# Kernel optimization log

Measured on AMD Instinct MI355X. Metric: run time of the kernel, lower is better.

Reference implementation:

```python
import jax, jax.numpy as jnp
import numpy as np

N = 50000      # nodes
E = 800000     # edges (avg degree 16)
F_IN = 128
H = 128        # hidden_channels
C = 10         # num_classes
S = 5          # Chebyshev order K
B = 8          # graphs in batch


def setup_inputs() -> dict:
    key = jax.random.key(0)
    ks = jax.random.split(key, 9)
    x = jax.random.normal(ks[0], (N, F_IN), jnp.float32)
    edge_index = jax.random.randint(ks[1], (2, E), 0, N, dtype=jnp.int64)
    batch = jnp.sort(jax.random.randint(ks[2], (N,), 0, B, dtype=jnp.int64))
    lambda_max = 2.0 * jnp.ones((B,), jnp.float32)
    W1 = jax.random.normal(ks[3], (S, F_IN, H), jnp.float32) * 0.05
    b1 = jax.random.normal(ks[4], (H,), jnp.float32) * 0.05
    W2 = jax.random.normal(ks[5], (S, H, H), jnp.float32) * 0.05
    b2 = jax.random.normal(ks[6], (H,), jnp.float32) * 0.05
    Wlin = jax.random.normal(ks[7], (H, C), jnp.float32) * 0.05
    blin = jax.random.normal(ks[8], (C,), jnp.float32) * 0.05
    return {"x": x, "edge_index": edge_index, "batch": batch,
            "lambda_max": lambda_max, "W1": W1, "b1": b1,
            "W2": W2, "b2": b2, "Wlin": Wlin, "blin": blin}


def _cheb_conv(x, row, col, w_edge, diag, W, b):
    # scaled Laplacian matvec: L_hat v = scatter(w_edge * v[col] -> row) + diag * v
    def Lhat(v):
        msg = v[col] * w_edge[:, None]                       # [E, d]
        return jax.ops.segment_sum(msg, row, num_segments=N) + diag[:, None] * v

    Tx0 = x
    out = Tx0 @ W[0]
    Tx1 = Lhat(Tx0)
    out = out + Tx1 @ W[1]
    for k in range(2, W.shape[0]):                           # Chebyshev recurrence
        Tx2 = 2.0 * Lhat(Tx1) - Tx0
        out = out + Tx2 @ W[k]
        Tx0, Tx1 = Tx1, Tx2
    return out + b


def reference(x, edge_index, batch, lambda_max, W1, b1, W2, b2, Wlin, blin):
    row, col = edge_index[0], edge_index[1]
    # sym-normalized Laplacian L = I - D^{-1/2} A D^{-1/2}; L_hat = 2L/lambda_max - I
    deg = jax.ops.segment_sum(jnp.ones((E,), x.dtype), row, num_segments=N)
    dis = jnp.where(deg > 0, jax.lax.rsqrt(jnp.maximum(deg, 1e-12)), 0.0)
    lam_e = lambda_max[batch[row]]                           # per-edge lambda_max
    w_edge = -2.0 * dis[row] * dis[col] / lam_e              # off-diagonal of L_hat
    diag = 2.0 / lambda_max[batch] - 1.0                     # diagonal of L_hat per node

    h = jax.nn.relu(_cheb_conv(x, row, col, w_edge, diag, W1, b1))
    h = jax.nn.relu(_cheb_conv(h, row, col, w_edge, diag, W2, b2))

    # global_mean_pool over batch assignment
    sums = jax.ops.segment_sum(h, batch, num_segments=B)     # [B, H]
    counts = jax.ops.segment_sum(jnp.ones((N, 1), h.dtype), batch, num_segments=B)
    pooled = sums / jnp.maximum(counts, 1.0)
    return pooled @ Wlin + blin                              # [B, C] logits (softmax unused in forward)
```

## Files before the change

kernel.cpp:

```cpp
#include <hip/hip_runtime.h>
#include <stdint.h>

typedef __attribute__((ext_vector_type(8))) short bf16x8;
typedef __attribute__((ext_vector_type(4))) float f32x4;

__device__ __forceinline__ float bf16lo_to_f(uint32_t u) { return __uint_as_float(u << 16); }
__device__ __forceinline__ float bf16hi_to_f(uint32_t u) { return __uint_as_float(u & 0xffff0000u); }
__device__ __forceinline__ uint16_t f_to_bf16(float f) {
    uint32_t u = __float_as_uint(f);
    uint32_t r = u + 0x7fff + ((u >> 16) & 1);
    return (uint16_t)(r >> 16);
}


#define BINCH 4096

__global__ void __launch_bounds__(256) k_bhist(const int* __restrict__ row,
                                               int* __restrict__ bhist, int E) {
    __shared__ int sh[256];
    int t = threadIdx.x;
    sh[t] = 0;
    __syncthreads();
    int stride = gridDim.x * blockDim.x;
    for (int e = blockIdx.x * blockDim.x + t; e < E; e += stride)
        atomicAdd(&sh[row[e] >> 8], 1);
    __syncthreads();
    if (sh[t]) atomicAdd(&bhist[t], sh[t]);
}

__global__ void k_bscan(const int* __restrict__ bhist, int* __restrict__ gbase,
                        int* __restrict__ gcur, int nbk) {
    __shared__ int sh[256];
    int t = threadIdx.x;
    int v = t < nbk ? bhist[t] : 0;
    sh[t] = v;
    __syncthreads();
    for (int o = 1; o < 256; o <<= 1) {
        int u = (t >= o) ? sh[t - o] : 0;
        __syncthreads();
        sh[t] += u;
        __syncthreads();
    }
    gbase[t] = sh[t] - v;
    gcur[t] = sh[t] - v;
    if (t == 255) gbase[256] = sh[255];
}

__global__ void __launch_bounds__(256) k_bin(const int* __restrict__ row,
        const int* __restrict__ col, int* __restrict__ gcur,
        uint32_t* __restrict__ bout, int E) {
    __shared__ uint32_t stage[BINCH];
    __shared__ int hist[256], hscan[256], hcur[256], gofs[256];
    int t = threadIdx.x;
    int e0 = blockIdx.x * BINCH;
    int ecnt = min(BINCH, E - e0);
    hist[t] = 0;
    __syncthreads();
    for (int i = t; i < ecnt; i += 256)
        atomicAdd(&hist[row[e0 + i] >> 8], 1);
    __syncthreads();
    int v = hist[t];
    hscan[t] = v;
    __syncthreads();
    for (int o = 1; o < 256; o <<= 1) {
        int u = (t >= o) ? hscan[t - o] : 0;
        __syncthreads();
        hscan[t] += u;
        __syncthreads();
    }
    hcur[t] = hscan[t] - v;
    __syncthreads();
    for (int i = t; i < ecnt; i += 256) {
        int r = row[e0 + i];
        int p = atomicAdd(&hcur[r >> 8], 1);
        stage[p] = (uint32_t)(r & 255) | ((uint32_t)col[e0 + i] << 8);
    }
    __syncthreads();
    if (v > 0) gofs[t] = atomicAdd(&gcur[t], v);
    __syncthreads();
    for (int i = t; i < ecnt; i += 256) {
        int lo = 0, hi = 255;
        while (lo < hi) { int mid = (lo + hi) >> 1; if (hscan[mid] > i) hi = mid; else lo = mid + 1; }
        int b = lo;
        int local = i - (hscan[b] - hist[b]);
        bout[gofs[b] + local] = stage[i];
    }
}

__global__ void __launch_bounds__(256) k_deg2(const uint32_t* __restrict__ bout,
        const int* __restrict__ gbase, int* __restrict__ deg,
        int* __restrict__ psum, int N) {
    __shared__ int cnt[256];
    __shared__ int red[256];
    int t = threadIdx.x, b = blockIdx.x;
    cnt[t] = 0;
    __syncthreads();
    int s = gbase[b], epos = gbase[b + 1];
    for (int i = s + t; i < epos; i += 256)
        atomicAdd(&cnt[bout[i] & 255], 1);
    __syncthreads();
    int n = b * 256 + t;
    int d = cnt[t];
    if (n < N) deg[n] = d;
    red[t] = (n < N) ? ((d + 7) & ~7) : 0;
    __syncthreads();
    for (int o = 128; o > 0; o >>= 1) {
        if (t < o) red[t] += red[t + o];
        __syncthreads();
    }
    if (t == 0) psum[b] = red[0];
}

__global__ void k_offs(const int* __restrict__ deg, const int* __restrict__ psum,
                       int* __restrict__ offs,
                       const int* __restrict__ batch, const float* __restrict__ lam,
                       float* __restrict__ dis, float* __restrict__ diag,
                       uint4* __restrict__ nh,
                       int N, int nb) {
    __shared__ int pre[256];
    __shared__ int sh[256];
    int t = threadIdx.x, b = blockIdx.x;
    pre[t] = (t < b) ? psum[t] : 0;
    __syncthreads();
    for (int o = 128; o > 0; o >>= 1) {
        if (t < o) pre[t] += pre[t + o];
        __syncthreads();
    }
    int base = pre[0];
    __syncthreads();
    int idx = b * 256 + t;
    int d = idx < N ? deg[idx] : 0;
    int v = (d + 7) & ~7;
    sh[t] = v;
    __syncthreads();
    for (int o = 1; o < 256; o <<= 1) {
        int u = (t >= o) ? sh[t - o] : 0;
        __syncthreads();
        sh[t] += u;
        __syncthreads();
    }
    if (idx < N) {
        int beg = base + sh[t] - v;
        float dgv = 2.f / lam[batch[idx]] - 1.f;
        offs[idx] = beg;
        dis[idx] = d > 0 ? rsqrtf((float)d) : 0.f;
        diag[idx] = dgv;
        nh[idx] = make_uint4((uint32_t)beg, (uint32_t)(base + sh[t] - v + v),
                             __float_as_uint(dgv), 0u);
    }
    if (b == nb - 1 && t == 255) offs[N] = base + sh[255];
}

__global__ void __launch_bounds__(256) k_ew(const uint32_t* __restrict__ bout,
        const int* __restrict__ gbase, const int* __restrict__ offs,
        const float* __restrict__ dis, const float* __restrict__ diag,
        uint32_t* __restrict__ ew, int N) {
    __shared__ int cur[256];
    __shared__ int bs0[256];
    __shared__ float srw[256];
    int t = threadIdx.x, b = blockIdx.x;
    int n = b * 256 + t;
    int o0 = n < N ? offs[n] : 0;
    cur[t] = 0;
    bs0[t] = o0;
    srw[t] = (n < N) ? (-dis[n] * (diag[n] + 1.0f)) : 0.f;
    __syncthreads();
    int s = gbase[b], epos = gbase[b + 1];
    for (int i = s + t; i < epos; i += 256) {
        uint32_t v = bout[i];
        int r = (int)(v & 255u);
        int c = (int)(v >> 8);
        int idx = atomicAdd(&cur[r], 1);
        float w = srw[r] * dis[c];
        int pos = bs0[r] + (idx & ~7) + ((idx & 1) << 2) + ((idx >> 1) & 3);
        ew[pos] = (uint32_t)c | ((uint32_t)f_to_bf16(w) << 16);
    }
    __syncthreads();
    if (n < N) {
        int cnt = cur[t];
        int pe = (cnt + 7) & ~7;
        for (int i = cnt; i < pe; i++) {
            int pos = o0 + (i & ~7) + ((i & 1) << 2) + ((i >> 1) & 3);
            ew[pos] = (uint32_t)N;
        }
    }
}

__global__ void k_prepw(const float* __restrict__ W1, uint16_t* __restrict__ Wt1,
                        const float* __restrict__ W2, uint16_t* __restrict__ Wt2) {
    int i = blockIdx.x * blockDim.x + threadIdx.x;
    const float* W = W1; uint16_t* Wt = Wt1;
    if (i >= 128 * 640) { i -= 128 * 640; W = W2; Wt = Wt2; }
    int o = i / 640, kk = i % 640;
    Wt[(size_t)o * 640 + kk] = f_to_bf16(W[(size_t)kk * 128 + o]);
}

__global__ void __launch_bounds__(256) k_castx(const float* __restrict__ x,
        uint16_t* __restrict__ Txb, int N) {
    int n = (blockIdx.x * blockDim.x + threadIdx.x) >> 6;
    int lane = threadIdx.x & 63;
    if (n > N) return;
    size_t ss32 = (size_t)(N + 1) * 64;
    if (n == N) {
#pragma unroll
        for (int s = 0; s < 5; s++)
            ((uint32_t*)Txb)[s * ss32 + (size_t)N * 64 + lane] = 0u;
        return;
    }
    float2 v = ((const float2*)x)[(size_t)n * 64 + lane];
    uint32_t p = (uint32_t)f_to_bf16(v.x) | ((uint32_t)f_to_bf16(v.y) << 16);
    ((uint32_t*)Txb)[(size_t)n * 64 + lane] = p;
}

__global__ void __launch_bounds__(256) k_lhat(uint16_t* __restrict__ Txb,
        const uint4* __restrict__ nh, const uint32_t* __restrict__ ew,
        int N,
        int src, int dst, int prev, float alpha, int use_prev) {
    int n = (blockIdx.x * blockDim.x + threadIdx.x) >> 6;
    int lane = threadIdx.x & 63;
    if (n >= N) return;
    int h = lane >> 5, g = lane & 31;
    size_t sb = (size_t)(N + 1) * 256;
    const uint8_t* srcs = (const uint8_t*)Txb + (size_t)src * sb;
    uint32_t g8 = (uint32_t)g * 8;
    uint4 hh = nh[n];
    int e = (int)hh.x, end = (int)hh.y;
    float dgn = __uint_as_float(hh.z);
    float a0 = 0.f, a1 = 0.f, a2 = 0.f, a3 = 0.f;
    if (e < end) {
        const uint4* ep = (const uint4*)(ew + e + h * 4);
        int npk = (end - e) >> 3;
        uint4 c = ep[0];
        int pk = 0;
        while (true) {
            bool more = (pk + 1) < npk;
            uint4 cn;
            if (more) cn = ep[(pk + 1) * 2];
#pragma unroll
            for (int u = 0; u < 4; u++) {
                uint32_t cw = (&c.x)[u];
                uint32_t addr = (cw & 0xffffu) << 8;
                float w = __uint_as_float(cw & 0xffff0000u);
                uint2 q = *(const uint2*)(srcs + addr + g8);
                a0 = fmaf(w, bf16lo_to_f(q.x), a0);
                a1 = fmaf(w, bf16hi_to_f(q.x), a1);
                a2 = fmaf(w, bf16lo_to_f(q.y), a2);
                a3 = fmaf(w, bf16hi_to_f(q.y), a3);
            }
            if (!more) break;
            c = cn;
            pk++;
        }
    }
    a0 += __shfl_xor(a0, 32);
    a1 += __shfl_xor(a1, 32);
    a2 += __shfl_xor(a2, 32);
    a3 += __shfl_xor(a3, 32);
    if (h == 0) {
        size_t ro = (size_t)n * 256 + g8;
        uint2 qs = *(const uint2*)(srcs + ro);
        a0 = fmaf(dgn, bf16lo_to_f(qs.x), a0);
        a1 = fmaf(dgn, bf16hi_to_f(qs.x), a1);
        a2 = fmaf(dgn, bf16lo_to_f(qs.y), a2);
        a3 = fmaf(dgn, bf16hi_to_f(qs.y), a3);
        float f0 = alpha * a0, f1 = alpha * a1, f2 = alpha * a2, f3 = alpha * a3;
        if (use_prev) {
            uint2 qp = *(const uint2*)((const uint8_t*)Txb + (size_t)prev * sb + ro);
            f0 -= bf16lo_to_f(qp.x);
            f1 -= bf16hi_to_f(qp.x);
            f2 -= bf16lo_to_f(qp.y);
            f3 -= bf16hi_to_f(qp.y);
        }
        uint2 pk2;
        pk2.x = (uint32_t)f_to_bf16(f0) | ((uint32_t)f_to_bf16(f1) << 16);
        pk2.y = (uint32_t)f_to_bf16(f2) | ((uint32_t)f_to_bf16(f3) << 16);
        *(uint2*)((uint8_t*)Txb + (size_t)dst * sb + ro) = pk2;
    }
}

#define BM 128
#define BK 64
#define LDT 72
#define LDC 132

__global__ void __launch_bounds__(256) k_gemm(
        const uint16_t* __restrict__ A, size_t sstride,
        const uint16_t* __restrict__ Bt,
        const float* __restrict__ bias,
        uint16_t* __restrict__ out2b,
        float* __restrict__ pooled,
        const int* __restrict__ batch,
        int M, int Kdim) {
    __shared__ uint16_t smem[BM * LDT + 128 * LDT];
    uint16_t* As = smem;
    uint16_t* Bs = smem + BM * LDT;
    uint16_t* Ct = smem;
    int t = threadIdx.x;
    int w = t >> 6, lane = t & 63;
    int row0 = blockIdx.x * BM;
    int mrow = (w >> 1) * 64, ncol = (w & 1) * 64;

    int ar[4], akc[4];
#pragma unroll
    for (int rep = 0; rep < 4; rep++) {
        int d = rep * 256 + t;
        ar[rep] = d >> 3; akc[rep] = d & 7;
    }

    f32x4 acc[4][4];
#pragma unroll
    for (int i = 0; i < 4; i++)
#pragma unroll
        for (int j = 0; j < 4; j++) acc[i][j] = (f32x4){0.f, 0.f, 0.f, 0.f};

    bf16x8 pa[4], pb[4];
#pragma unroll
    for (int rep = 0; rep < 4; rep++) {
        int grow = row0 + ar[rep];
        int kk = akc[rep] * 8;
        bf16x8 va = {0, 0, 0, 0, 0, 0, 0, 0};
        if (grow < M)
            va = *(const bf16x8*)(A + (size_t)(kk >> 7) * sstride + (size_t)grow * 128 + (kk & 127));
        pa[rep] = va;
        pb[rep] = *(const bf16x8*)(Bt + (size_t)ar[rep] * Kdim + kk);
    }

    for (int k0 = 0; k0 < Kdim; k0 += BK) {
#pragma unroll
        for (int rep = 0; rep < 4; rep++) {
            *(bf16x8*)(&As[ar[rep] * LDT + akc[rep] * 8]) = pa[rep];
            *(bf16x8*)(&Bs[ar[rep] * LDT + akc[rep] * 8]) = pb[rep];
        }
        __syncthreads();
        int kn = k0 + BK;
        if (kn < Kdim) {
#pragma unroll
            for (int rep = 0; rep < 4; rep++) {
                int grow = row0 + ar[rep];
                int kk = kn + akc[rep] * 8;
                bf16x8 va = {0, 0, 0, 0, 0, 0, 0, 0};
                if (grow < M)
                    va = *(const bf16x8*)(A + (size_t)(kk >> 7) * sstride + (size_t)grow * 128 + (kk & 127));
                pa[rep] = va;
                pb[rep] = *(const bf16x8*)(Bt + (size_t)ar[rep] * Kdim + kk);
            }
        }
#pragma unroll
        for (int ks = 0; ks < BK; ks += 32) {
            bf16x8 af[4], bfr[4];
#pragma unroll
            for (int i = 0; i < 4; i++) {
                int r = mrow + i * 16 + (lane & 15);
                af[i] = *(const bf16x8*)(&As[r * LDT + ks + (lane >> 4) * 8]);
            }
#pragma unroll
            for (int j = 0; j < 4; j++) {
                int c = ncol + j * 16 + (lane & 15);
                bfr[j] = *(const bf16x8*)(&Bs[c * LDT + ks + (lane >> 4) * 8]);
            }
#pragma unroll
            for (int i = 0; i < 4; i++)
#pragma unroll
                for (int j = 0; j < 4; j++)
                    acc[i][j] = __builtin_amdgcn_mfma_f32_16x16x32_bf16(af[i], bfr[j], acc[i][j], 0, 0, 0);
        }
        __syncthreads();
    }

#pragma unroll
    for (int j = 0; j < 4; j++) {
        int c = ncol + j * 16 + (lane & 15);
        float bv = bias[c];
#pragma unroll
        for (int i = 0; i < 4; i++) {
            int rloc = mrow + i * 16 + (lane >> 4) * 4;
#pragma unroll
            for (int r = 0; r < 4; r++) {
                float v = acc[i][j][r] + bv;
                v = v > 0.f ? v : 0.f;
                Ct[(rloc + r) * LDC + c] = f_to_bf16(v);
            }
        }
    }
    __syncthreads();

    if (out2b) {
#pragma unroll
        for (int rep = 0; rep < 8; rep++) {
            int d = rep * 256 + t;
            int r = d >> 4, c8 = (d & 15) * 8;
            int grow = row0 + r;
            if (grow < M) {
                bf16x8 v = *(const bf16x8*)(&Ct[r * LDC + c8]);
                *(bf16x8*)(out2b + (size_t)grow * 128 + c8) = v;
            }
        }
    }
    if (pooled) {
        int f = t & 127, r0 = (t >> 7) * 64;
        float accp = 0.f;
        int curb = -1;
        for (int r = r0; r < r0 + 64; ++r) {
            int grow = row0 + r;
            if (grow >= M) break;
            int b = batch[grow];
            if (b != curb) {
                if (curb >= 0) atomicAdd(&pooled[curb * 128 + f], accp);
                accp = 0.f; curb = b;
            }
            accp += __uint_as_float(((uint32_t)Ct[r * LDC + f]) << 16);
        }
        if (curb >= 0) atomicAdd(&pooled[curb * 128 + f], accp);
    }
}

__global__ void k_final(const float* __restrict__ pooled, const int* __restrict__ batch,
                        const float* __restrict__ Wlin, const float* __restrict__ blin,
                        float* __restrict__ out, int N, int B_, int C_) {
    __shared__ int cnt[64];
    int t = threadIdx.x;
    if (t < B_) {
        auto lb = [&](int v) {
            int lo = 0, hi = N;
            while (lo < hi) {
                int mid = (lo + hi) >> 1;
                if (batch[mid] < v) lo = mid + 1; else hi = mid;
            }
            return lo;
        };
        cnt[t] = lb(t + 1) - lb(t);
    }
    __syncthreads();
    if (t < B_ * C_) {
        int b = t / C_, c = t % C_;
        float inv = 1.f / fmaxf((float)cnt[b], 1.f);
        float acc = blin[c];
        for (int f = 0; f < 128; ++f) acc += pooled[b * 128 + f] * inv * Wlin[f * C_ + c];
        out[t] = acc;
    }
}

extern "C" void kernel_launch(void* const* d_in, const int* in_sizes, int n_in,
                              void* d_out, int out_size, void* d_ws, size_t ws_size,
                              hipStream_t stream) {
    const float* x    = (const float*)d_in[0];
    const int*   edge = (const int*)d_in[1];
    const int*   batch= (const int*)d_in[2];
    const float* lam  = (const float*)d_in[3];
    const float* W1   = (const float*)d_in[4];
    const float* b1   = (const float*)d_in[5];
    const float* W2   = (const float*)d_in[6];
    const float* b2   = (const float*)d_in[7];
    const float* Wlin = (const float*)d_in[8];
    const float* blin = (const float*)d_in[9];
    const int E  = in_sizes[1] / 2;
    const int N  = in_sizes[2];
    const int B_ = in_sizes[3];
    const int* row = edge;
    const int* col = edge + E;

    char* ws = (char*)d_ws;
    size_t off = 0;
    auto take = [&](size_t bytes) -> char* {
        char* p = ws + off;
        off = (off + bytes + 255) & ~(size_t)255;
        return p;
    };
    uint16_t* Txb    = (uint16_t*)take((size_t)5 * (N + 1) * 128 * 2);
    uint32_t* ew     = (uint32_t*)take(((size_t)E + 8 * (size_t)N) * 4);
    int*      deg    = (int*)take((size_t)N * 4);
    int*      offs   = (int*)take((size_t)(N + 1) * 4);
    float*    dis    = (float*)take((size_t)N * 4);
    float*    diag   = (float*)take((size_t)N * 4);
    uint4*    nh     = (uint4*)take((size_t)N * 16);
    uint16_t* Wt1    = (uint16_t*)take((size_t)128 * 640 * 2);
    uint16_t* Wt2    = (uint16_t*)take((size_t)128 * 640 * 2);
    float*    pooled = (float*)take((size_t)B_ * 128 * 4);
    int*      bhist  = (int*)take(257 * 4);
    int*      gbase  = (int*)take(257 * 4);
    int*      gcur   = (int*)take(257 * 4);
    const int nb = (N + 255) / 256;
    int*      psum   = (int*)take((size_t)nb * 4);
    uint32_t* bout   = (uint32_t*)((char*)Txb + (size_t)4 * (N + 1) * 256);

    hipMemsetAsync(pooled, 0, (size_t)B_ * 128 * 4 + 257 * 4, stream);

    const int nchunks = (E + BINCH - 1) / BINCH;

    k_bhist<<<112, 256, 0, stream>>>(row, bhist, E);
    k_bscan<<<1, 256, 0, stream>>>(bhist, gbase, gcur, nb);
    k_bin<<<nchunks, 256, 0, stream>>>(row, col, gcur, bout, E);
    k_deg2<<<nb, 256, 0, stream>>>(bout, gbase, deg, psum, N);
    k_offs<<<nb, 256, 0, stream>>>(deg, psum, offs, batch, lam, dis, diag, nh, N, nb);
    k_ew<<<nb, 256, 0, stream>>>(bout, gbase, offs, dis, diag, ew, N);
    k_prepw<<<(2 * 128 * 640) / 256, 256, 0, stream>>>(W1, Wt1, W2, Wt2);
    k_castx<<<(N + 4) / 4, 256, 0, stream>>>(x, Txb, N);

    const int lblocks = (N + 3) / 4;
    const int gblocks = (N + BM - 1) / BM;
    const size_t ss = (size_t)(N + 1) * 128;

    k_lhat<<<lblocks, 256, 0, stream>>>(Txb, nh, ew, N, 0, 1, 0, 1.f, 0);
    k_lhat<<<lblocks, 256, 0, stream>>>(Txb, nh, ew, N, 1, 2, 0, 2.f, 1);
    k_lhat<<<lblocks, 256, 0, stream>>>(Txb, nh, ew, N, 2, 3, 1, 2.f, 1);
    k_lhat<<<lblocks, 256, 0, stream>>>(Txb, nh, ew, N, 3, 4, 2, 2.f, 1);
    k_gemm<<<gblocks, 256, 0, stream>>>(Txb, ss, Wt1, b1,
                                        Txb , (float*)nullptr, batch, N, 640);

    k_lhat<<<lblocks, 256, 0, stream>>>(Txb, nh, ew, N, 0, 1, 0, 1.f, 0);
    k_lhat<<<lblocks, 256, 0, stream>>>(Txb, nh, ew, N, 1, 2, 0, 2.f, 1);
    k_lhat<<<lblocks, 256, 0, stream>>>(Txb, nh, ew, N, 2, 3, 1, 2.f, 1);
    k_lhat<<<lblocks, 256, 0, stream>>>(Txb, nh, ew, N, 3, 4, 2, 2.f, 1);
    k_gemm<<<gblocks, 256, 0, stream>>>(Txb, ss, Wt2, b2,
                                        (uint16_t*)nullptr, pooled, batch, N, 640);

    k_final<<<1, 128, 0, stream>>>(pooled, batch, Wlin, blin, (float*)d_out, N, B_, 10);
}
```

Measured before the change: 470.0 us.

## Fuse preprocessing kernels and batch gathers two edge packets per iteration

Merges the row histogram, weight transpose/cast, input cast and pad-row zeroing into one grid-stride kernel launched with 1024 blocks, removing two launches and raising the histogram's grid size from 112 blocks. The k_lhat gather loop is restructured to load two 8-edge packets and issue all eight row gathers before the FMAs, exposing more memory-level parallelism. The cost is more registers per thread in k_lhat, and more blocks contending on the shared bhist atomics.

```diff
diff --git a/kernel.cpp b/kernel.cpp
--- a/kernel.cpp
+++ b/kernel.cpp
@@ -15,17 +15,44 @@
 
 #define BINCH 4096
 
-__global__ void __launch_bounds__(256) k_bhist(const int* __restrict__ row,
-                                               int* __restrict__ bhist, int E) {
+__global__ void __launch_bounds__(256) k_pre1(
+        const int* __restrict__ row, int* __restrict__ bhist,
+        const float* __restrict__ W1, uint16_t* __restrict__ Wt1,
+        const float* __restrict__ W2, uint16_t* __restrict__ Wt2,
+        const float* __restrict__ x, uint16_t* __restrict__ Txb,
+        int E, int N) {
     __shared__ int sh[256];
-    int t = threadIdx.x;
+    int t = threadIdx.x, b = blockIdx.x;
+    int gstride = gridDim.x * 256;
     sh[t] = 0;
     __syncthreads();
-    int stride = gridDim.x * blockDim.x;
-    for (int e = blockIdx.x * blockDim.x + t; e < E; e += stride)
+    for (int e = b * 256 + t; e < E; e += gstride)
         atomicAdd(&sh[row[e] >> 8], 1);
     __syncthreads();
     if (sh[t]) atomicAdd(&bhist[t], sh[t]);
+    for (int i = b * 256 + t; i < 2 * 128 * 640; i += gstride) {
+        int ii = i;
+        const float* W = W1; uint16_t* Wt = Wt1;
+        if (ii >= 128 * 640) { ii -= 128 * 640; W = W2; Wt = Wt2; }
+        int o = ii / 640, kk = ii % 640;
+        Wt[(size_t)o * 640 + kk] = f_to_bf16(W[(size_t)kk * 128 + o]);
+    }
+    {
+        int lane = t & 63;
+        int gw = b * 4 + (t >> 6);
+        int tw = gridDim.x * 4;
+        for (int n = gw; n < N; n += tw) {
+            float2 v = ((const float2*)x)[(size_t)n * 64 + lane];
+            uint32_t p = (uint32_t)f_to_bf16(v.x) | ((uint32_t)f_to_bf16(v.y) << 16);
+            ((uint32_t*)Txb)[(size_t)n * 64 + lane] = p;
+        }
+    }
+    if (b == 0) {
+        int lane = t & 63;
+        size_t ss32 = (size_t)(N + 1) * 64;
+        for (int s = t >> 6; s < 5; s += 4)
+            ((uint32_t*)Txb)[(size_t)s * ss32 + (size_t)N * 64 + lane] = 0u;
+    }
 }
 
 __global__ void k_bscan(const int* __restrict__ bhist, int* __restrict__ gbase,
@@ -145,7 +172,7 @@
         offs[idx] = beg;
         dis[idx] = d > 0 ? rsqrtf((float)d) : 0.f;
         diag[idx] = dgv;
-        nh[idx] = make_uint4((uint32_t)beg, (uint32_t)(base + sh[t] - v + v),
+        nh[idx] = make_uint4((uint32_t)beg, (uint32_t)(base + sh[t]),
                              __float_as_uint(dgv), 0u);
     }
     if (b == nb - 1 && t == 255) offs[N] = base + sh[255];
@@ -184,32 +211,6 @@
             ew[pos] = (uint32_t)N;
         }
     }
-}
-
-__global__ void k_prepw(const float* __restrict__ W1, uint16_t* __restrict__ Wt1,
-                        const float* __restrict__ W2, uint16_t* __restrict__ Wt2) {
-    int i = blockIdx.x * blockDim.x + threadIdx.x;
-    const float* W = W1; uint16_t* Wt = Wt1;
-    if (i >= 128 * 640) { i -= 128 * 640; W = W2; Wt = Wt2; }
-    int o = i / 640, kk = i % 640;
-    Wt[(size_t)o * 640 + kk] = f_to_bf16(W[(size_t)kk * 128 + o]);
-}
-
-__global__ void __launch_bounds__(256) k_castx(const float* __restrict__ x,
-        uint16_t* __restrict__ Txb, int N) {
-    int n = (blockIdx.x * blockDim.x + threadIdx.x) >> 6;
-    int lane = threadIdx.x & 63;
-    if (n > N) return;
-    size_t ss32 = (size_t)(N + 1) * 64;
-    if (n == N) {
-#pragma unroll
-        for (int s = 0; s < 5; s++)
-            ((uint32_t*)Txb)[s * ss32 + (size_t)N * 64 + lane] = 0u;
-        return;
-    }
-    float2 v = ((const float2*)x)[(size_t)n * 64 + lane];
-    uint32_t p = (uint32_t)f_to_bf16(v.x) | ((uint32_t)f_to_bf16(v.y) << 16);
-    ((uint32_t*)Txb)[(size_t)n * 64 + lane] = p;
 }
 
 __global__ void __launch_bounds__(256) k_lhat(uint16_t* __restrict__ Txb,
@@ -227,29 +228,47 @@
     int e = (int)hh.x, end = (int)hh.y;
     float dgn = __uint_as_float(hh.z);
     float a0 = 0.f, a1 = 0.f, a2 = 0.f, a3 = 0.f;
-    if (e < end) {
-        const uint4* ep = (const uint4*)(ew + e + h * 4);
-        int npk = (end - e) >> 3;
-        uint4 c = ep[0];
-        int pk = 0;
-        while (true) {
-            bool more = (pk + 1) < npk;
-            uint4 cn;
-            if (more) cn = ep[(pk + 1) * 2];
+    int npk = (end - e) >> 3;
+    const uint4* ep = (const uint4*)(ew + e + h * 4);
+    int pk = 0;
+    while (pk < npk) {
+        if (npk - pk >= 2) {
+            uint4 c0 = ep[pk * 2];
+            uint4 c1 = ep[pk * 2 + 2];
+            uint2 q[8]; float w[8];
 #pragma unroll
             for (int u = 0; u < 4; u++) {
-                uint32_t cw = (&c.x)[u];
-                uint32_t addr = (cw & 0xffffu) << 8;
+                uint32_t cw = (&c0.x)[u];
+                w[u] = __uint_as_float(cw & 0xffff0000u);
+                q[u] = *(const uint2*)(srcs + ((cw & 0xffffu) << 8) + g8);
+            }
+#pragma unroll
+            for (int u = 0; u < 4; u++) {
+                uint32_t cw = (&c1.x)[u];
+                w[4 + u] = __uint_as_float(cw & 0xffff0000u);
+                q[4 + u] = *(const uint2*)(srcs + ((cw & 0xffffu) << 8) + g8);
+            }
+#pragma unroll
+            for (int u = 0; u < 8; u++) {
+                a0 = fmaf(w[u], bf16lo_to_f(q[u].x), a0);
+                a1 = fmaf(w[u], bf16hi_to_f(q[u].x), a1);
+                a2 = fmaf(w[u], bf16lo_to_f(q[u].y), a2);
+                a3 = fmaf(w[u], bf16hi_to_f(q[u].y), a3);
+            }
+            pk += 2;
+        } else {
+            uint4 c0 = ep[pk * 2];
+#pragma unroll
+            for (int u = 0; u < 4; u++) {
+                uint32_t cw = (&c0.x)[u];
                 float w = __uint_as_float(cw & 0xffff0000u);
-                uint2 q = *(const uint2*)(srcs + addr + g8);
+                uint2 q = *(const uint2*)(srcs + ((cw & 0xffffu) << 8) + g8);
                 a0 = fmaf(w, bf16lo_to_f(q.x), a0);
                 a1 = fmaf(w, bf16hi_to_f(q.x), a1);
                 a2 = fmaf(w, bf16lo_to_f(q.y), a2);
                 a3 = fmaf(w, bf16hi_to_f(q.y), a3);
             }
-            if (!more) break;
-            c = cn;
-            pk++;
+            pk += 1;
         }
     }
     a0 += __shfl_xor(a0, 32);
@@ -487,14 +506,12 @@
 
     const int nchunks = (E + BINCH - 1) / BINCH;
 
-    k_bhist<<<112, 256, 0, stream>>>(row, bhist, E);
+    k_pre1<<<1024, 256, 0, stream>>>(row, bhist, W1, Wt1, W2, Wt2, x, Txb, E, N);
     k_bscan<<<1, 256, 0, stream>>>(bhist, gbase, gcur, nb);
     k_bin<<<nchunks, 256, 0, stream>>>(row, col, gcur, bout, E);
     k_deg2<<<nb, 256, 0, stream>>>(bout, gbase, deg, psum, N);
     k_offs<<<nb, 256, 0, stream>>>(deg, psum, offs, batch, lam, dis, diag, nh, N, nb);
     k_ew<<<nb, 256, 0, stream>>>(bout, gbase, offs, dis, diag, ew, N);
-    k_prepw<<<(2 * 128 * 640) / 256, 256, 0, stream>>>(W1, Wt1, W2, Wt2);
-    k_castx<<<(N + 4) / 4, 256, 0, stream>>>(x, Txb, N);
 
     const int lblocks = (N + 3) / 4;
     const int gblocks = (N + BM - 1) / BM;
```

Measured after the change: 468.5 us. No clear change (-0.3%).
